# Optimization experiments

Measured on AMD Instinct MI355X. Metric: run time of the kernel, lower is better.

## Reference

```python
import jax, jax.numpy as jnp
import numpy as np

H = W = 128      # image_shape
B = 64           # batch_size
O = 32           # orbit_size
RADIANS = True   # args.radians
RADIAN_INIT = 1.57
AFFINE_INIT = 0.1


def setup_inputs() -> dict:
    key = jax.random.key(0)
    k1, k2 = jax.random.split(key)
    X = jax.random.normal(k1, (B, H * W), dtype=jnp.float32)
    eps = jax.random.uniform(k2, (O, 7), dtype=jnp.float32)
    base = np.array([3.14, 1.0, 1.0, 1.0, 1.0, 1.0, 1.0], np.float32)
    ident = np.array([RADIAN_INIT, 1.0, 1.0, 0.0, 0.0, 0.0, 0.0], np.float32)
    tmin = ident - AFFINE_INIT * base
    tmax = np.array([-RADIAN_INIT, 1.0, 1.0, 0.0, 0.0, 0.0, 0.0], np.float32) + AFFINE_INIT * base
    return {
        "X": X,
        "eps": eps,
        "theta_min": jnp.asarray(tmin)[None, :],
        "theta_max": jnp.asarray(tmax)[None, :],
    }


def _affine_entries(thetas):
    # thetas: [O, 7] = [angle, sx, sy, shear_x, shear_y, tx, ty]
    # A = R(angle) @ [[sx, px], [py, sy]]  (rotation * scale/shear), t = [tx, ty]
    ang, sx, sy, px, py, tx, ty = (thetas[:, i] for i in range(7))
    if not RADIANS:
        ang = ang * (np.pi / 180.0)
    c, s = jnp.cos(ang), jnp.sin(ang)
    a00 = c * sx - s * py
    a01 = c * px - s * sy
    a10 = s * sx + c * py
    a11 = s * px + c * sy
    return a00, a01, a10, a11, tx, ty


def reference(X, eps, theta_min, theta_max):
    # sample orbit thetas: [O, 7]
    thetas = theta_min + (theta_max - theta_min) * eps
    a00, a01, a10, a11, tx, ty = _affine_entries(thetas)

    imgs = X.reshape(-1, H, W)  # [B, H, W]

    # normalized sampling grid in [-1, 1]
    xg = jnp.linspace(-1.0, 1.0, W, dtype=X.dtype)
    yg = jnp.linspace(-1.0, 1.0, H, dtype=X.dtype)
    Yg, Xg = jnp.meshgrid(yg, xg, indexing="ij")  # [H, W]

    # affine-transformed source coords per orbit sample: [O, H, W]
    xs = a00[:, None, None] * Xg + a01[:, None, None] * Yg + tx[:, None, None]
    ys = a10[:, None, None] * Xg + a11[:, None, None] * Yg + ty[:, None, None]

    # to pixel coords (align-corners convention)
    x = (xs + 1.0) * (W - 1) * 0.5
    y = (ys + 1.0) * (H - 1) * 0.5

    x0f = jnp.floor(x)
    y0f = jnp.floor(y)
    wx = x - x0f
    wy = y - y0f
    x0 = jnp.clip(x0f.astype(jnp.int32), 0, W - 1)
    x1 = jnp.clip(x0f.astype(jnp.int32) + 1, 0, W - 1)
    y0 = jnp.clip(y0f.astype(jnp.int32), 0, H - 1)
    y1 = jnp.clip(y0f.astype(jnp.int32) + 1, 0, H - 1)

    # gather 4 corners: fancy index over all images at once -> [B, O, H, W]
    Ia = imgs[:, y0, x0]
    Ib = imgs[:, y1, x0]
    Ic = imgs[:, y0, x1]
    Id = imgs[:, y1, x1]

    wa = (1.0 - wx) * (1.0 - wy)
    wb = (1.0 - wx) * wy
    wc = wx * (1.0 - wy)
    wd = wx * wy

    out = Ia * wa + Ib * wb + Ic * wc + Id * wd  # [B, O, H, W]
    out = jnp.transpose(out, (1, 0, 2, 3))       # [O, B, H, W]: per-theta batches
    return out.reshape(B * O, H, W, 1)
```

## Files before the change

### kernel.cpp

```cpp
#include <hip/hip_runtime.h>

#define HH 128
#define WW 128
#define BB 64
#define OO 32

__global__ void coeff_kernel(const float* __restrict__ eps,
                             const float* __restrict__ tmin,
                             const float* __restrict__ tmax,
                             float* __restrict__ coef) {
    int o = threadIdx.x;
    if (o >= OO) return;
    float th[7];
#pragma unroll
    for (int i = 0; i < 7; ++i) {
        float mn = tmin[i], mx = tmax[i];
        th[i] = mn + (mx - mn) * eps[o * 7 + i];
    }
    float ang = th[0], sx = th[1], sy = th[2], px = th[3], py = th[4], tx = th[5], ty = th[6];
    float c = cosf(ang), s = sinf(ang);
    float a00 = c * sx - s * py;
    float a01 = c * px - s * sy;
    float a10 = s * sx + c * py;
    float a11 = s * px + c * sy;
    const float half = 0.5f * (WW - 1);
    coef[o * 8 + 0] = a00 * half;
    coef[o * 8 + 1] = a01 * half;
    coef[o * 8 + 2] = (tx + 1.0f) * half;
    coef[o * 8 + 3] = a10 * half;
    coef[o * 8 + 4] = a11 * half;
    coef[o * 8 + 5] = (ty + 1.0f) * half;
}

__launch_bounds__(512)
__global__ void sample_kernel(const float* __restrict__ X,
                              const float* __restrict__ coef,
                              float* __restrict__ out) {
    __shared__ float img[HH * WW];

    const int bid = blockIdx.x;
    const int og  = bid & 7;
    const int b   = bid >> 3;
    const int tid = threadIdx.x;

    {
        const float4* __restrict__ src = (const float4*)(X + b * (HH * WW));
        float4* dst = (float4*)img;
#pragma unroll
        for (int i = 0; i < 8; ++i)
            dst[tid + i * 512] = src[tid + i * 512];
    }
    __syncthreads();

    const int w  = tid & (WW - 1);
    const int h0 = tid >> 7;
    const float step = 2.0f / 127.0f;
    const float Xg = -1.0f + w * step;
    const float hi = 126.999992f;

#pragma unroll
    for (int j = 0; j < 4; ++j) {
        const int o = og * 4 + j;
        const float cx0 = coef[o * 8 + 0];
        const float cx1 = coef[o * 8 + 1];
        const float cxt = coef[o * 8 + 2];
        const float cy0 = coef[o * 8 + 3];
        const float cy1 = coef[o * 8 + 4];
        const float cyt = coef[o * 8 + 5];

        const float bxw = fmaf(cx0, Xg, cxt);
        const float byw = fmaf(cy0, Xg, cyt);

        float* __restrict__ outp = out + ((size_t)(o * BB + b) * (HH * WW)) + w;

#pragma unroll 8
        for (int i = 0; i < 32; ++i) {
            const int h = h0 + i * 4;
            const float Yg = -1.0f + h * step;
            float x = fmaf(cx1, Yg, bxw);
            float y = fmaf(cy1, Yg, byw);
            x = fminf(fmaxf(x, 0.0f), hi);
            y = fminf(fmaxf(y, 0.0f), hi);

            const float x0f = floorf(x);
            const float y0f = floorf(y);
            const float wx = x - x0f;
            const float wy = y - y0f;
            const int idx = ((int)y0f << 7) + (int)x0f;

            const float Ia = img[idx];
            const float Ic = img[idx + 1];
            const float Ib = img[idx + WW];
            const float Id = img[idx + WW + 1];

            const float top = fmaf(wx, Ic - Ia, Ia);
            const float bot = fmaf(wx, Id - Ib, Ib);
            outp[h * WW] = fmaf(wy, bot - top, top);
        }
    }
}

extern "C" void kernel_launch(void* const* d_in, const int* in_sizes, int n_in,
                              void* d_out, int out_size, void* d_ws, size_t ws_size,
                              hipStream_t stream) {
    const float* X    = (const float*)d_in[0];
    const float* eps  = (const float*)d_in[1];
    const float* tmin = (const float*)d_in[2];
    const float* tmax = (const float*)d_in[3];
    float* out  = (float*)d_out;
    float* coef = (float*)d_ws;

    coeff_kernel<<<1, 64, 0, stream>>>(eps, tmin, tmax, coef);

    const int nblocks = BB * 8;
    sample_kernel<<<nblocks, 512, 0, stream>>>(X, coef, out);
}
```

Baseline: 158.3 us.

## Fuse coefficient computation into sampler and use 1024-thread blocks with incremental coords

```diff
diff --git a/kernel.cpp b/kernel.cpp
--- a/kernel.cpp
+++ b/kernel.cpp
@@ -5,88 +5,84 @@
 #define BB 64
 #define OO 32
 
-__global__ void coeff_kernel(const float* __restrict__ eps,
-                             const float* __restrict__ tmin,
-                             const float* __restrict__ tmax,
-                             float* __restrict__ coef) {
-    int o = threadIdx.x;
-    if (o >= OO) return;
-    float th[7];
-#pragma unroll
-    for (int i = 0; i < 7; ++i) {
-        float mn = tmin[i], mx = tmax[i];
-        th[i] = mn + (mx - mn) * eps[o * 7 + i];
-    }
-    float ang = th[0], sx = th[1], sy = th[2], px = th[3], py = th[4], tx = th[5], ty = th[6];
-    float c = cosf(ang), s = sinf(ang);
-    float a00 = c * sx - s * py;
-    float a01 = c * px - s * sy;
-    float a10 = s * sx + c * py;
-    float a11 = s * px + c * sy;
-    const float half = 0.5f * (WW - 1);
-    coef[o * 8 + 0] = a00 * half;
-    coef[o * 8 + 1] = a01 * half;
-    coef[o * 8 + 2] = (tx + 1.0f) * half;
-    coef[o * 8 + 3] = a10 * half;
-    coef[o * 8 + 4] = a11 * half;
-    coef[o * 8 + 5] = (ty + 1.0f) * half;
-}
-
-__launch_bounds__(512)
+__launch_bounds__(1024, 8)
 __global__ void sample_kernel(const float* __restrict__ X,
-                              const float* __restrict__ coef,
+                              const float* __restrict__ eps,
+                              const float* __restrict__ tmin,
+                              const float* __restrict__ tmax,
                               float* __restrict__ out) {
     __shared__ float img[HH * WW];
+    __shared__ float scoef[4][6];
 
     const int bid = blockIdx.x;
     const int og  = bid & 7;
     const int b   = bid >> 3;
     const int tid = threadIdx.x;
 
+    if (tid < 4) {
+        const int o = og * 4 + tid;
+        float th[7];
+#pragma unroll
+        for (int i = 0; i < 7; ++i) {
+            const float mn = tmin[i], mx = tmax[i];
+            th[i] = mn + (mx - mn) * eps[o * 7 + i];
+        }
+        const float ang = th[0], sx = th[1], sy = th[2], px = th[3],
+                    py = th[4], tx = th[5], ty = th[6];
+        const float c = cosf(ang), s = sinf(ang);
+        const float half = 0.5f * (WW - 1);
+        scoef[tid][0] = (c * sx - s * py) * half;
+        scoef[tid][1] = (c * px - s * sy) * half;
+        scoef[tid][2] = (tx + 1.0f) * half;
+        scoef[tid][3] = (s * sx + c * py) * half;
+        scoef[tid][4] = (s * px + c * sy) * half;
+        scoef[tid][5] = (ty + 1.0f) * half;
+    }
+
     {
         const float4* __restrict__ src = (const float4*)(X + b * (HH * WW));
         float4* dst = (float4*)img;
 #pragma unroll
-        for (int i = 0; i < 8; ++i)
-            dst[tid + i * 512] = src[tid + i * 512];
+        for (int i = 0; i < 4; ++i)
+            dst[tid + i * 1024] = src[tid + i * 1024];
     }
     __syncthreads();
 
     const int w  = tid & (WW - 1);
     const int h0 = tid >> 7;
-    const float step = 2.0f / 127.0f;
-    const float Xg = -1.0f + w * step;
-    const float hi = 126.999992f;
+    const float step  = 2.0f / 127.0f;
+    const float hstep = 8.0f * step;
+    const float Xg  = -1.0f + w * step;
+    const float Yg0 = -1.0f + h0 * step;
+    const float hi  = 126.999992f;
 
 #pragma unroll
     for (int j = 0; j < 4; ++j) {
         const int o = og * 4 + j;
-        const float cx0 = coef[o * 8 + 0];
-        const float cx1 = coef[o * 8 + 1];
-        const float cxt = coef[o * 8 + 2];
-        const float cy0 = coef[o * 8 + 3];
-        const float cy1 = coef[o * 8 + 4];
-        const float cyt = coef[o * 8 + 5];
+        const float cx0 = scoef[j][0];
+        const float cx1 = scoef[j][1];
+        const float cxt = scoef[j][2];
+        const float cy0 = scoef[j][3];
+        const float cy1 = scoef[j][4];
+        const float cyt = scoef[j][5];
 
-        const float bxw = fmaf(cx0, Xg, cxt);
-        const float byw = fmaf(cy0, Xg, cyt);
+        float x = fmaf(cx1, Yg0, fmaf(cx0, Xg, cxt));
+        float y = fmaf(cy1, Yg0, fmaf(cy0, Xg, cyt));
+        const float dx = cx1 * hstep;
+        const float dy = cy1 * hstep;
 
-        float* __restrict__ outp = out + ((size_t)(o * BB + b) * (HH * WW)) + w;
+        float* __restrict__ outp =
+            out + ((size_t)(o * BB + b) * (HH * WW)) + h0 * WW + w;
 
-#pragma unroll 8
-        for (int i = 0; i < 32; ++i) {
-            const int h = h0 + i * 4;
-            const float Yg = -1.0f + h * step;
-            float x = fmaf(cx1, Yg, bxw);
-            float y = fmaf(cy1, Yg, byw);
-            x = fminf(fmaxf(x, 0.0f), hi);
-            y = fminf(fmaxf(y, 0.0f), hi);
-
-            const float x0f = floorf(x);
-            const float y0f = floorf(y);
-            const float wx = x - x0f;
-            const float wy = y - y0f;
-            const int idx = ((int)y0f << 7) + (int)x0f;
+#pragma unroll
+        for (int i = 0; i < 16; ++i) {
+            const float xc = __builtin_amdgcn_fmed3f(x, 0.0f, hi);
+            const float yc = __builtin_amdgcn_fmed3f(y, 0.0f, hi);
+            const float x0f = floorf(xc);
+            const float y0f = floorf(yc);
+            const float wx = xc - x0f;
+            const float wy = yc - y0f;
+            const int idx = (int)fmaf(y0f, 128.0f, x0f);
 
             const float Ia = img[idx];
             const float Ic = img[idx + 1];
@@ -95,7 +91,11 @@
 
             const float top = fmaf(wx, Ic - Ia, Ia);
             const float bot = fmaf(wx, Id - Ib, Ib);
-            outp[h * WW] = fmaf(wy, bot - top, top);
+            *outp = fmaf(wy, bot - top, top);
+
+            outp += 8 * WW;
+            x += dx;
+            y += dy;
         }
     }
 }
@@ -107,11 +107,8 @@
     const float* eps  = (const float*)d_in[1];
     const float* tmin = (const float*)d_in[2];
     const float* tmax = (const float*)d_in[3];
-    float* out  = (float*)d_out;
-    float* coef = (float*)d_ws;
-
-    coeff_kernel<<<1, 64, 0, stream>>>(eps, tmin, tmax, coef);
+    float* out = (float*)d_out;
 
     const int nblocks = BB * 8;
-    sample_kernel<<<nblocks, 512, 0, stream>>>(X, coef, out);
+    sample_kernel<<<nblocks, 1024, 0, stream>>>(X, eps, tmin, tmax, out);
 }
```

Result: faster. 153.8 us (-2.8%).
